# Kernel tuning notes

Measured on AMD Instinct MI355X. Metric: run time of the kernel, lower is better.

The kernel has to match this reference:

```python
import jax, jax.numpy as jnp
import numpy as np

L, P = 16384, 512
DT_MIN, DT_MAX = 0.001, 0.1
THRESHOLD = 1.0  # spike threshold assumed for cartesian_spike


def setup_inputs() -> dict:
    key = jax.random.key(0)
    k1, k2, k3, k4, k5, k6 = jax.random.split(key, 6)
    u = jax.random.normal(k1, (L, P), dtype=jnp.float32)
    # Stored Lambda param: [..., 0] = log(-Re(Lambda)) with Re(Lambda) < 0, [..., 1] = Im(Lambda)
    lam_real_neg = jax.random.uniform(k2, (P,), minval=0.1, maxval=1.0)  # -Re(Lambda)
    lam_imag = jax.random.normal(k3, (P,)) * 3.0
    Lambda = jnp.stack([jnp.log(lam_real_neg), lam_imag], axis=-1).astype(jnp.float32)
    # init_log_steps: log(dt) uniform in [log(dt_min), log(dt_max)], shape (P, 1)
    log_step = (np.log(DT_MIN) + jax.random.uniform(k4, (P, 1)) * (np.log(DT_MAX) - np.log(DT_MIN))).astype(jnp.float32)
    V_re = jax.random.normal(k5, (P, P), dtype=jnp.float32) / np.sqrt(P)
    V_im = jax.random.normal(k6, (P, P), dtype=jnp.float32) / np.sqrt(P)
    return {"u": u, "Lambda": Lambda, "log_step": log_step, "V_re": V_re, "V_im": V_im}


def _binop(q_i, q_j):
    A_i, b_i = q_i
    A_j, b_j = q_j
    return (A_j * A_i, A_j * b_i + b_j)


def reference(u, Lambda, log_step, V_re, V_im):
    # keep_imag = False: u stays real. discretization = 'zoh', activation = 'cartesian_spike'.
    Lambda_tilde = -jnp.exp(Lambda[..., 0]) + 1j * Lambda[..., 1]            # (P,) complex
    step = jnp.exp(log_step[:, 0])                                            # (P,)
    Lambda_bar = jnp.exp(Lambda_tilde * step)                                 # (P,) |.|<1
    # B_tilde = I, so zoh gives B_bar = diag((Lambda_bar - 1)/Lambda); B_bar @ u_t = coef * u_t
    B_coef = (Lambda_bar - 1.0) / Lambda_tilde                                # (P,)
    Lambda_elements = jnp.broadcast_to(Lambda_bar, (u.shape[0], Lambda_bar.shape[0]))
    Bu_elements = B_coef[None, :] * u.astype(Lambda_bar.dtype)                # (L, P) complex
    _, xs = jax.lax.associative_scan(_binop, (Lambda_elements, Bu_elements))  # (L, P)
    V = V_re + 1j * V_im
    xs = xs @ V.T                                                             # vmap(V @ x) over L
    spikes = (xs.real > THRESHOLD).astype(jnp.float32)                        # cartesian_spike
    return spikes
```

## Files before the change

kernel.cpp:

```cpp
#include <hip/hip_runtime.h>

#define L_LEN   16384
#define P_DIM   512
#define CHUNK   128
#define NCHUNK  128

#define KDIM    1024
#define NDIM    512
#define BM      128
#define BN      128
#define BK      64

typedef __bf16 bf16_t;
typedef __bf16 bf16x8 __attribute__((ext_vector_type(8)));
typedef float  floatx4 __attribute__((ext_vector_type(4)));

__device__ __forceinline__ void channel_consts(const float* __restrict__ Lam,
                                               const float* __restrict__ lstep,
                                               int p, float& ar, float& ai,
                                               float& br, float& bi) {
    float lr = -expf(Lam[2 * p + 0]);
    float li = Lam[2 * p + 1];
    float s  = expf(lstep[p]);
    float er = expf(lr * s);
    ar = er * cosf(li * s);
    ai = er * sinf(li * s);
    float dr = ar - 1.0f, di = ai;
    float inv = 1.0f / (lr * lr + li * li);
    br = (dr * lr + di * li) * inv;
    bi = (di * lr - dr * li) * inv;
}

__global__ void __launch_bounds__(P_DIM) k_scan_ends(const float* __restrict__ u,
        const float* __restrict__ Lam, const float* __restrict__ lstep,
        float2* __restrict__ endv) {
    int p = threadIdx.x;
    int c = blockIdx.x;
    float ar, ai, br, bi;
    channel_consts(Lam, lstep, p, ar, ai, br, bi);
    float xr = 0.f, xi = 0.f;
    const float* up = u + (size_t)c * CHUNK * P_DIM + p;
    #pragma unroll 8
    for (int k = 0; k < CHUNK; ++k) {
        float uv = up[(size_t)k * P_DIM];
        float nr = ar * xr - ai * xi + br * uv;
        float ni = ar * xi + ai * xr + bi * uv;
        xr = nr; xi = ni;
    }
    endv[c * P_DIM + p] = make_float2(xr, xi);
}

__global__ void __launch_bounds__(P_DIM) k_carry(const float* __restrict__ Lam,
        const float* __restrict__ lstep, const float2* __restrict__ endv,
        float2* __restrict__ carry) {
    int p = threadIdx.x;
    float lr = -expf(Lam[2 * p + 0]);
    float li = Lam[2 * p + 1];
    float s  = expf(lstep[p]);
    float t  = s * (float)CHUNK;
    float er = expf(lr * t);
    float Ar = er * cosf(li * t);
    float Ai = er * sinf(li * t);
    float xr = 0.f, xi = 0.f;
    #pragma unroll 4
    for (int c = 0; c < NCHUNK; ++c) {
        carry[c * P_DIM + p] = make_float2(xr, xi);
        float2 e = endv[c * P_DIM + p];
        float nr = Ar * xr - Ai * xi + e.x;
        float ni = Ar * xi + Ai * xr + e.y;
        xr = nr; xi = ni;
    }
}

__global__ void __launch_bounds__(P_DIM) k_materialize(const float* __restrict__ u,
        const float* __restrict__ Lam, const float* __restrict__ lstep,
        const float2* __restrict__ carry, bf16_t* __restrict__ A) {
    int p = threadIdx.x;
    int c = blockIdx.x;
    float ar, ai, br, bi;
    channel_consts(Lam, lstep, p, ar, ai, br, bi);
    float2 x0 = carry[c * P_DIM + p];
    float xr = x0.x, xi = x0.y;
    const float* up = u + (size_t)c * CHUNK * P_DIM + p;
    bf16_t* Ap = A + (size_t)c * CHUNK * KDIM;
    #pragma unroll 4
    for (int k = 0; k < CHUNK; ++k) {
        float uv = up[(size_t)k * P_DIM];
        float nr = ar * xr - ai * xi + br * uv;
        float ni = ar * xi + ai * xr + bi * uv;
        xr = nr; xi = ni;
        Ap[(size_t)k * KDIM + p]         = (bf16_t)xr;
        Ap[(size_t)k * KDIM + P_DIM + p] = (bf16_t)xi;
    }
}

__global__ void __launch_bounds__(256) k_bt(const float* __restrict__ Vre,
        const float* __restrict__ Vim, bf16_t* __restrict__ Bt) {
    int idx = blockIdx.x * 256 + threadIdx.x;
    int j = idx >> 10;
    int k = idx & 1023;
    float v = (k < P_DIM) ? Vre[j * P_DIM + k] : -Vim[j * P_DIM + (k - P_DIM)];
    Bt[idx] = (bf16_t)v;
}

__global__ void __launch_bounds__(256) k_gemm(const bf16_t* __restrict__ A,
        const bf16_t* __restrict__ Bt, float* __restrict__ out) {
    __shared__ uint4 As4[BM * BK * 2 / 16];
    __shared__ uint4 Bs4[BN * BK * 2 / 16];

    const int tid  = threadIdx.x;
    const int lane = tid & 63;
    const int w    = tid >> 6;
    const int m0   = blockIdx.x * BM;
    const int n0   = blockIdx.y * BN;
    const int wm   = (w >> 1) * 64;
    const int wn   = (w & 1) * 64;

    const int fr_m = lane & 15;
    const int fr_g = lane >> 4;

    floatx4 acc[4][4];
    #pragma unroll
    for (int i = 0; i < 4; ++i)
        #pragma unroll
        for (int j = 0; j < 4; ++j) {
            floatx4 z = {0.f, 0.f, 0.f, 0.f};
            acc[i][j] = z;
        }

    const bf16_t* Asrc = A  + (size_t)m0 * KDIM;
    const bf16_t* Bsrc = Bt + (size_t)n0 * KDIM;

    for (int kt = 0; kt < KDIM; kt += BK) {
        __syncthreads();
        #pragma unroll
        for (int i = 0; i < 4; ++i) {
            int q   = i * 256 + tid;
            int row = q >> 3;
            int sc  = q & 7;
            int gc  = sc ^ (row & 7);
            As4[q] = *((const uint4*)(Asrc + (size_t)row * KDIM + kt) + gc);
            Bs4[q] = *((const uint4*)(Bsrc + (size_t)row * KDIM + kt) + gc);
        }
        __syncthreads();
        #pragma unroll
        for (int kk = 0; kk < BK; kk += 32) {
            bf16x8 af[4], bf[4];
            #pragma unroll
            for (int i = 0; i < 4; ++i) {
                int m  = wm + i * 16 + fr_m;
                int cc = (kk >> 3) + fr_g;
                int sc = cc ^ (m & 7);
                af[i] = *(const bf16x8*)((const bf16_t*)As4 + m * BK + sc * 8);
            }
            #pragma unroll
            for (int j = 0; j < 4; ++j) {
                int n  = wn + j * 16 + fr_m;
                int cc = (kk >> 3) + fr_g;
                int sc = cc ^ (n & 7);
                bf[j] = *(const bf16x8*)((const bf16_t*)Bs4 + n * BK + sc * 8);
            }
            #pragma unroll
            for (int i = 0; i < 4; ++i)
                #pragma unroll
                for (int j = 0; j < 4; ++j)
                    acc[i][j] = __builtin_amdgcn_mfma_f32_16x16x32_bf16(
                        af[i], bf[j], acc[i][j], 0, 0, 0);
        }
    }

    #pragma unroll
    for (int i = 0; i < 4; ++i)
        #pragma unroll
        for (int j = 0; j < 4; ++j)
            #pragma unroll
            for (int r = 0; r < 4; ++r) {
                int rr = wm + i * 16 + fr_g * 4 + r;
                int cl = wn + j * 16 + fr_m;
                float v = acc[i][j][r];
                out[(size_t)(m0 + rr) * NDIM + (n0 + cl)] = (v > 1.0f) ? 1.0f : 0.0f;
            }
}

extern "C" void kernel_launch(void* const* d_in, const int* in_sizes, int n_in,
                              void* d_out, int out_size, void* d_ws, size_t ws_size,
                              hipStream_t stream) {
    (void)in_sizes; (void)n_in; (void)out_size; (void)ws_size;
    const float* u     = (const float*)d_in[0];
    const float* Lam   = (const float*)d_in[1];
    const float* lstep = (const float*)d_in[2];
    const float* Vre   = (const float*)d_in[3];
    const float* Vim   = (const float*)d_in[4];
    float* out = (float*)d_out;

    char* ws = (char*)d_ws;
    const size_t endv_bytes  = (size_t)NCHUNK * P_DIM * sizeof(float2);
    const size_t carry_bytes = endv_bytes;
    const size_t bt_bytes    = (size_t)NDIM * KDIM * sizeof(bf16_t);
    float2* endv  = (float2*)(ws);
    float2* carry = (float2*)(ws + endv_bytes);
    bf16_t* Bt    = (bf16_t*)(ws + endv_bytes + carry_bytes);
    bf16_t* A     = (bf16_t*)(ws + endv_bytes + carry_bytes + bt_bytes);

    hipLaunchKernelGGL(k_scan_ends, dim3(NCHUNK), dim3(P_DIM), 0, stream,
                       u, Lam, lstep, endv);
    hipLaunchKernelGGL(k_bt, dim3(NDIM * KDIM / 256), dim3(256), 0, stream,
                       Vre, Vim, Bt);
    hipLaunchKernelGGL(k_carry, dim3(1), dim3(P_DIM), 0, stream,
                       Lam, lstep, endv, carry);
    hipLaunchKernelGGL(k_materialize, dim3(NCHUNK), dim3(P_DIM), 0, stream,
                       u, Lam, lstep, carry, A);
    hipLaunchKernelGGL(k_gemm, dim3(L_LEN / BM, NDIM / BN), dim3(256), 0, stream,
                       A, Bt, out);
}
```

Baseline: 154.2 us.

## Halve scan chunk, interleave re/im bf16 writes, use direct global-to-LDS loads in GEMM

Scan chunk length drops to 64 with 256 chunks, giving the scan and materialize kernels more blocks in parallel while making the serial carry pass longer. Real and imaginary parts are now interleaved along K and written as packed 32-bit words in both the materialized A and the transposed V, which keeps the GEMM correct because both operands share the permutation. The GEMM tile load now uses global_load_lds to copy straight into shared memory without passing through registers. The workspace offsets are fixed at MB boundaries.

New measurement: 155.6 us. No clear change (+0.9%).

```diff
diff --git a/kernel.cpp b/kernel.cpp
--- a/kernel.cpp
+++ b/kernel.cpp
@@ -2,8 +2,8 @@
 
 #define L_LEN   16384
 #define P_DIM   512
-#define CHUNK   128
-#define NCHUNK  128
+#define CHUNK   64
+#define NCHUNK  256
 
 #define KDIM    1024
 #define NDIM    512
@@ -62,7 +62,7 @@
     float Ar = er * cosf(li * t);
     float Ai = er * sinf(li * t);
     float xr = 0.f, xi = 0.f;
-    #pragma unroll 4
+    #pragma unroll 8
     for (int c = 0; c < NCHUNK; ++c) {
         carry[c * P_DIM + p] = make_float2(xr, xi);
         float2 e = endv[c * P_DIM + p];
@@ -70,6 +70,17 @@
         float ni = Ar * xi + Ai * xr + e.y;
         xr = nr; xi = ni;
     }
+}
+
+__global__ void __launch_bounds__(256) k_bt(const float* __restrict__ Vre,
+        const float* __restrict__ Vim, bf16_t* __restrict__ Bt) {
+    int idx = blockIdx.x * 256 + threadIdx.x;
+    int j = idx >> 9;
+    int c = idx & 511;
+    union { unsigned int w; bf16_t h[2]; } pk;
+    pk.h[0] = (bf16_t)Vre[j * P_DIM + c];
+    pk.h[1] = (bf16_t)(-Vim[j * P_DIM + c]);
+    ((unsigned int*)Bt)[idx] = pk.w;
 }
 
 __global__ void __launch_bounds__(P_DIM) k_materialize(const float* __restrict__ u,
@@ -82,31 +93,24 @@
     float2 x0 = carry[c * P_DIM + p];
     float xr = x0.x, xi = x0.y;
     const float* up = u + (size_t)c * CHUNK * P_DIM + p;
-    bf16_t* Ap = A + (size_t)c * CHUNK * KDIM;
-    #pragma unroll 4
-    for (int k = 0; k < CHUNK; ++k) {
-        float uv = up[(size_t)k * P_DIM];
+    unsigned int* Ap32 = (unsigned int*)(A + (size_t)c * CHUNK * KDIM);
+    #pragma unroll 8
+    for (int t = 0; t < CHUNK; ++t) {
+        float uv = up[(size_t)t * P_DIM];
         float nr = ar * xr - ai * xi + br * uv;
         float ni = ar * xi + ai * xr + bi * uv;
         xr = nr; xi = ni;
-        Ap[(size_t)k * KDIM + p]         = (bf16_t)xr;
-        Ap[(size_t)k * KDIM + P_DIM + p] = (bf16_t)xi;
-    }
-}
-
-__global__ void __launch_bounds__(256) k_bt(const float* __restrict__ Vre,
-        const float* __restrict__ Vim, bf16_t* __restrict__ Bt) {
-    int idx = blockIdx.x * 256 + threadIdx.x;
-    int j = idx >> 10;
-    int k = idx & 1023;
-    float v = (k < P_DIM) ? Vre[j * P_DIM + k] : -Vim[j * P_DIM + (k - P_DIM)];
-    Bt[idx] = (bf16_t)v;
+        union { unsigned int w; bf16_t h[2]; } pk;
+        pk.h[0] = (bf16_t)xr;
+        pk.h[1] = (bf16_t)xi;
+        Ap32[(size_t)t * (KDIM / 2) + p] = pk.w;
+    }
 }
 
 __global__ void __launch_bounds__(256) k_gemm(const bf16_t* __restrict__ A,
         const bf16_t* __restrict__ Bt, float* __restrict__ out) {
-    __shared__ uint4 As4[BM * BK * 2 / 16];
-    __shared__ uint4 Bs4[BN * BK * 2 / 16];
+    __shared__ __align__(16) bf16_t As[BM * BK];
+    __shared__ __align__(16) bf16_t Bs[BN * BK];
 
     const int tid  = threadIdx.x;
     const int lane = tid & 63;
@@ -115,7 +119,6 @@
     const int n0   = blockIdx.y * BN;
     const int wm   = (w >> 1) * 64;
     const int wn   = (w & 1) * 64;
-
     const int fr_m = lane & 15;
     const int fr_g = lane >> 4;
 
@@ -135,37 +138,45 @@
         __syncthreads();
         #pragma unroll
         for (int i = 0; i < 4; ++i) {
-            int q   = i * 256 + tid;
-            int row = q >> 3;
-            int sc  = q & 7;
-            int gc  = sc ^ (row & 7);
-            As4[q] = *((const uint4*)(Asrc + (size_t)row * KDIM + kt) + gc);
-            Bs4[q] = *((const uint4*)(Bsrc + (size_t)row * KDIM + kt) + gc);
+            const int cb = i * 256 + w * 64;
+            const int c  = cb + lane;
+            const int r  = c >> 3;
+            const int gc = (c & 7) ^ (r & 7);
+            const bf16_t* ga = Asrc + (size_t)r * KDIM + kt + gc * 8;
+            const bf16_t* gb = Bsrc + (size_t)r * KDIM + kt + gc * 8;
+            __builtin_amdgcn_global_load_lds(
+                (const __attribute__((address_space(1))) unsigned int*)ga,
+                (__attribute__((address_space(3))) unsigned int*)((char*)As + cb * 16),
+                16, 0, 0);
+            __builtin_amdgcn_global_load_lds(
+                (const __attribute__((address_space(1))) unsigned int*)gb,
+                (__attribute__((address_space(3))) unsigned int*)((char*)Bs + cb * 16),
+                16, 0, 0);
         }
         __syncthreads();
+
         #pragma unroll
         for (int kk = 0; kk < BK; kk += 32) {
-            bf16x8 af[4], bf[4];
+            const int kc = (kk >> 3) + fr_g;
+            bf16x8 af[4], bfv[4];
             #pragma unroll
             for (int i = 0; i < 4; ++i) {
-                int m  = wm + i * 16 + fr_m;
-                int cc = (kk >> 3) + fr_g;
-                int sc = cc ^ (m & 7);
-                af[i] = *(const bf16x8*)((const bf16_t*)As4 + m * BK + sc * 8);
+                int m = wm + i * 16 + fr_m;
+                af[i] = *(const bf16x8*)((const char*)As + m * (BK * 2)
+                                         + ((kc ^ (m & 7)) << 4));
             }
             #pragma unroll
             for (int j = 0; j < 4; ++j) {
-                int n  = wn + j * 16 + fr_m;
-                int cc = (kk >> 3) + fr_g;
-                int sc = cc ^ (n & 7);
-                bf[j] = *(const bf16x8*)((const bf16_t*)Bs4 + n * BK + sc * 8);
+                int n = wn + j * 16 + fr_m;
+                bfv[j] = *(const bf16x8*)((const char*)Bs + n * (BK * 2)
+                                          + ((kc ^ (n & 7)) << 4));
             }
             #pragma unroll
             for (int i = 0; i < 4; ++i)
                 #pragma unroll
                 for (int j = 0; j < 4; ++j)
                     acc[i][j] = __builtin_amdgcn_mfma_f32_16x16x32_bf16(
-                        af[i], bf[j], acc[i][j], 0, 0, 0);
+                        af[i], bfv[j], acc[i][j], 0, 0, 0);
         }
     }
 
@@ -177,8 +188,8 @@
             for (int r = 0; r < 4; ++r) {
                 int rr = wm + i * 16 + fr_g * 4 + r;
                 int cl = wn + j * 16 + fr_m;
-                float v = acc[i][j][r];
-                out[(size_t)(m0 + rr) * NDIM + (n0 + cl)] = (v > 1.0f) ? 1.0f : 0.0f;
+                out[(size_t)(m0 + rr) * NDIM + (n0 + cl)] =
+                    (acc[i][j][r] > 1.0f) ? 1.0f : 0.0f;
             }
 }
 
@@ -194,17 +205,14 @@
     float* out = (float*)d_out;
 
     char* ws = (char*)d_ws;
-    const size_t endv_bytes  = (size_t)NCHUNK * P_DIM * sizeof(float2);
-    const size_t carry_bytes = endv_bytes;
-    const size_t bt_bytes    = (size_t)NDIM * KDIM * sizeof(bf16_t);
     float2* endv  = (float2*)(ws);
-    float2* carry = (float2*)(ws + endv_bytes);
-    bf16_t* Bt    = (bf16_t*)(ws + endv_bytes + carry_bytes);
-    bf16_t* A     = (bf16_t*)(ws + endv_bytes + carry_bytes + bt_bytes);
+    float2* carry = (float2*)(ws + (1 << 20));
+    bf16_t* Bt    = (bf16_t*)(ws + (2 << 20));
+    bf16_t* A     = (bf16_t*)(ws + (4 << 20));
 
     hipLaunchKernelGGL(k_scan_ends, dim3(NCHUNK), dim3(P_DIM), 0, stream,
                        u, Lam, lstep, endv);
-    hipLaunchKernelGGL(k_bt, dim3(NDIM * KDIM / 256), dim3(256), 0, stream,
+    hipLaunchKernelGGL(k_bt, dim3(NDIM * P_DIM / 256), dim3(256), 0, stream,
                        Vre, Vim, Bt);
     hipLaunchKernelGGL(k_carry, dim3(1), dim3(P_DIM), 0, stream,
                        Lam, lstep, endv, carry);
```
